# Kernel tuning notes

Measured on AMD Instinct MI355X. Metric: run time of the kernel, lower is better.

Reference implementation:

```python
import jax, jax.numpy as jnp
import numpy as np

P = 32    # num_particles
B = 64    # batch_size
T = 100   # seq_len
W = 50    # window_length
E = 64    # act embedding dim (emb_obs=0)
H = 256   # hidden_dim
ALPHA = 0.5  # resamp_alpha


def setup_inputs() -> dict:
    key = jax.random.key(0)
    ks = jax.random.split(key, 12)
    def lin(k, fan_in, shape):
        return jax.random.normal(k, shape, jnp.float32) / np.sqrt(fan_in).astype(np.float32)
    u = jax.random.uniform(ks[4], (T, B, P, P), jnp.float32, 1e-6, 1.0 - 1e-6)
    return {
        "prev_window": jax.random.normal(ks[0], (B, T, W), jnp.float32),
        "h0": jax.random.uniform(ks[1], (P * B, H), jnp.float32),
        "c0": jax.random.uniform(ks[2], (P * B, H), jnp.float32),
        "eps": jax.random.normal(ks[3], (T, P * B, H), jnp.float32),
        "gumbel": -jnp.log(-jnp.log(u)),  # Gumbel noise for multinomial resampling
        "W_act": lin(ks[5], W, (W, E)), "b_act": jnp.zeros((E,), jnp.float32),
        "W_ih": lin(ks[6], E, (E, 5 * H)), "b_ih": jnp.zeros((5 * H,), jnp.float32),
        "W_hh": lin(ks[7], H, (H, 5 * H)), "b_hh": jnp.zeros((5 * H,), jnp.float32),
        "W_obs": lin(ks[8], H + E, (H + E, 1)), "b_obs": jnp.zeros((1,), jnp.float32),
        "W_lab": lin(ks[9], H, (H, 1)), "b_lab": jnp.zeros((1,), jnp.float32),
    }


def reference(prev_window, h0, c0, eps, gumbel, W_act, b_act, W_ih, b_ih,
              W_hh, b_hh, W_obs, b_obs, W_lab, b_lab):
    # act embedding, tiled over particles (particle-major, matching torch repeat)
    emb = jax.nn.relu(prev_window @ W_act + b_act)          # [B,T,E]
    xs = jnp.swapaxes(jnp.tile(emb, (P, 1, 1)), 0, 1)       # [T,P*B,E]
    p0 = jnp.full((P * B, 1), np.log(1.0 / P), jnp.float32)

    barange = jnp.arange(B)

    def step(carry, inputs):
        h, c, p = carry                                      # [PB,H],[PB,H],[PB,1]
        x, eps_t, g_t = inputs                               # [PB,E],[PB,H],[B,P,P]
        gates = x @ W_ih + b_ih + h @ W_hh + b_hh            # [PB,5H]
        i, f, g, o, var = jnp.split(gates, 5, axis=1)
        mu = jax.nn.sigmoid(f) * c + jax.nn.sigmoid(i) * jnp.tanh(g)
        c1 = mu + jax.nn.softplus(var) * eps_t               # stochastic cell (reparameterize)
        h1 = jax.nn.sigmoid(o) * jnp.tanh(c1)
        # observation log-likelihood per particle
        logpdf = jnp.concatenate([h1, x], axis=1) @ W_obs + b_obs  # [PB,1]
        p1 = jax.nn.log_softmax((p + logpdf).reshape(P, B), axis=0)  # [P,B]
        # soft resampling: q = alpha*w + (1-alpha)/P, sample via Gumbel-argmax
        w1 = jnp.exp(p1)
        logits = jnp.log(ALPHA * w1 + (1.0 - ALPHA) / P)     # [P_src,B]
        idx = jnp.argmax(logits.T[:, None, :] + g_t, axis=-1).T  # [P_new,B]
        h_new = h1.reshape(P, B, H)[idx, barange[None, :]]   # [P,B,H]
        c_new = c1.reshape(P, B, H)[idx, barange[None, :]]
        w = w1[idx, barange[None, :]]                        # [P,B]
        w = w / (ALPHA * w + (1.0 - ALPHA) / P)              # importance correction
        p_new = jax.nn.log_softmax(jnp.log(w), axis=0)
        h_new = h_new.reshape(P * B, H)
        c_new = c_new.reshape(P * B, H)
        p_new = p_new.reshape(P * B, 1)
        return (h_new, c_new, p_new), (h_new, p_new)

    _, (hs, ps) = jax.lax.scan(step, (h0, c0, p0), (xs, eps, gumbel))
    # hs: [T,PB,H], ps: [T,PB,1]; dropout rate 0 -> identity
    prob = ps.reshape(T, P, B, 1)
    out = hs.reshape(T, P, B, H)
    y = jnp.sum(out * jnp.exp(prob), axis=1)                 # weighted particle mean [T,B,H]
    y_out = jax.nn.sigmoid(y @ W_lab + b_lab)                # [T,B,1]
    pf_out = jax.nn.sigmoid(hs @ W_lab + b_lab)              # [T,PB,1]
    return y_out, pf_out
```

## Files before the change

### kernel.cpp

```cpp
#include <hip/hip_runtime.h>
#include <hip/hip_bf16.h>
#include <cstddef>
#include <cstdint>

#define PP 32
#define BB 64
#define TT 100
#define WW 50
#define EE 64
#define HH 256

typedef float f4 __attribute__((ext_vector_type(4)));
typedef __attribute__((ext_vector_type(8))) short short8;
typedef __attribute__((ext_vector_type(4))) float f32x4;

__device__ __forceinline__ float sigm(float x) { return 1.0f / (1.0f + expf(-x)); }
__device__ __forceinline__ float splus(float x) {
    return fmaxf(x, 0.0f) + log1pf(expf(-fabsf(x)));
}
__device__ __forceinline__ unsigned short bfh(float x) {
    __hip_bfloat16 h = __float2bfloat16(x);
    return *reinterpret_cast<unsigned short*>(&h);
}
__device__ __forceinline__ float bff(unsigned short u) {
    __hip_bfloat16 h; *reinterpret_cast<unsigned short*>(&h) = u;
    return __bfloat162float(h);
}

__global__ __launch_bounds__(256) void k_emb(
    const float* __restrict__ pw, const float* __restrict__ w_act,
    const float* __restrict__ b_act, const float* __restrict__ w_obs,
    const float* __restrict__ b_obs,
    unsigned short* __restrict__ embh, unsigned short* __restrict__ embl,
    float* __restrict__ xobs)
{
    int tid = threadIdx.x;
    int sub = tid >> 6;
    int e   = tid & 63;
    int bt  = blockIdx.x * 4 + sub;
    int b = bt / TT, t = bt % TT;

    __shared__ float pws[4][WW + 2];
    if (e < WW) pws[sub][e] = pw[(size_t)bt * WW + e];
    __syncthreads();

    float acc = b_act[e];
    #pragma unroll 5
    for (int w = 0; w < WW; ++w) acc += pws[sub][w] * w_act[w * EE + e];
    float r = fmaxf(acc, 0.0f);

    unsigned short uh = bfh(r);
    embh[((size_t)t * BB + b) * EE + e] = uh;
    embl[((size_t)t * BB + b) * EE + e] = bfh(r - bff(uh));

    float xv = r * w_obs[HH + e];
    #pragma unroll
    for (int d = 1; d < 64; d <<= 1) xv += __shfl_xor(xv, d);
    if (e == 0) xobs[t * BB + b] = xv + b_obs[0];
}

__global__ __launch_bounds__(256) void k_packB(
    const float* __restrict__ W_ih, const float* __restrict__ W_hh,
    unsigned short* __restrict__ Bp)
{
    int i = blockIdx.x * 256 + threadIdx.x;
    int colp = i / 51200;  int r = i - colp * 51200;
    int bidx = r / 2560;   r -= bidx * 2560;
    int g    = r / 512;    r -= g * 512;
    int lane = r >> 3;     int e = r & 7;

    int c = (bidx < 10) ? bidx : (bidx - 10);
    int k = c * 32 + (lane >> 4) * 8 + e;
    int col = g * HH + colp * 16 + (lane & 15);
    float w = (k < HH) ? W_hh[(size_t)k * 1280 + col]
                       : W_ih[(size_t)(k - HH) * 1280 + col];
    unsigned short uh = bfh(w);
    Bp[i] = (bidx < 10) ? uh : bfh(w - bff(uh));
}

__global__ __launch_bounds__(256) void k_split0(
    const float* __restrict__ h0, const float* __restrict__ c0,
    unsigned short* __restrict__ hh, unsigned short* __restrict__ hl,
    float* __restrict__ cc)
{
    int i = blockIdx.x * 256 + threadIdx.x;
    float v = h0[i];
    unsigned short uh = bfh(v);
    hh[i] = uh;
    hl[i] = bfh(v - bff(uh));
    cc[i] = c0[i];
}

__global__ __launch_bounds__(256, 2) void s1_mfma(
    const unsigned short* __restrict__ Bp,
    const unsigned short* __restrict__ embh_t, const unsigned short* __restrict__ embl_t,
    const unsigned short* __restrict__ hh_in, const unsigned short* __restrict__ hl_in,
    const float* __restrict__ c_in,
    unsigned short* __restrict__ hh_out, unsigned short* __restrict__ hl_out,
    float* __restrict__ c_out,
    const int* __restrict__ gidx,
    const float* __restrict__ b_ih, const float* __restrict__ b_hh,
    const float* __restrict__ w_obs, const float* __restrict__ w_lab,
    const float* __restrict__ eps_t,
    float* __restrict__ dpo, float* __restrict__ dpl)
{
    const int tid  = threadIdx.x;
    const int rp   = blockIdx.x >> 4;
    const int cp   = blockIdx.x & 15;
    const int lane = tid & 63;
    const int w    = tid >> 6;
    const int lh   = lane & 15;
    const int kq   = lane >> 4;
    const int R0   = rp * 64 + w * 16;

    const int myrow = R0 + lh;
    const int sr    = gidx ? gidx[myrow] : myrow;
    const size_t hoff = (size_t)sr * 512 + (size_t)kq * 16;
    const size_t eoff = (size_t)(myrow & 63) * 128 + (size_t)kq * 16;

    f32x4 acc[5];
    #pragma unroll
    for (int g = 0; g < 5; ++g) acc[g] = (f32x4)(0.0f);

    const char* hhp = (const char*)hh_in  + hoff;
    const char* hlp = (const char*)hl_in  + hoff;
    const char* ehp = (const char*)embh_t + eoff;
    const char* elp = (const char*)embl_t + eoff;
    const short8* bslab = (const short8*)Bp + (size_t)cp * 6400 + lane;

    #pragma unroll
    for (int cs = 0; cs < 10; ++cs) {
        short8 Ah, Al;
        if (cs < 8) {
            Ah = *(const short8*)(hhp + cs * 64);
            Al = *(const short8*)(hlp + cs * 64);
        } else {
            Ah = *(const short8*)(ehp + (cs - 8) * 64);
            Al = *(const short8*)(elp + (cs - 8) * 64);
        }
        short8 Bh[5], Bl[5];
        #pragma unroll
        for (int g = 0; g < 5; ++g) {
            Bh[g] = bslab[(cs * 5 + g) * 64];
            Bl[g] = bslab[((cs + 10) * 5 + g) * 64];
        }
        #pragma unroll
        for (int g = 0; g < 5; ++g)
            acc[g] = __builtin_amdgcn_mfma_f32_16x16x32_bf16(Ah, Bh[g], acc[g], 0, 0, 0);
        #pragma unroll
        for (int g = 0; g < 5; ++g)
            acc[g] = __builtin_amdgcn_mfma_f32_16x16x32_bf16(Ah, Bl[g], acc[g], 0, 0, 0);
        #pragma unroll
        for (int g = 0; g < 5; ++g)
            acc[g] = __builtin_amdgcn_mfma_f32_16x16x32_bf16(Al, Bh[g], acc[g], 0, 0, 0);
    }

    const int hcol = cp * 16 + lh;
    float bsum[5];
    #pragma unroll
    for (int g = 0; g < 5; ++g) bsum[g] = b_ih[g * HH + hcol] + b_hh[g * HH + hcol];
    const float wobs_l = w_obs[hcol];
    const float wlab_l = w_lab[hcol];

    #pragma unroll
    for (int reg = 0; reg < 4; ++reg) {
        int row = R0 + kq * 4 + reg;
        int sr2 = gidx ? gidx[row] : row;
        float cpv = c_in[(size_t)sr2 * HH + hcol];
        float ep  = eps_t[(size_t)row * HH + hcol];

        float gi = acc[0][reg] + bsum[0];
        float gf = acc[1][reg] + bsum[1];
        float gg = acc[2][reg] + bsum[2];
        float go = acc[3][reg] + bsum[3];
        float gv = acc[4][reg] + bsum[4];

        float mu  = sigm(gf) * cpv + sigm(gi) * tanhf(gg);
        float c1v = mu + splus(gv) * ep;
        float h1v = sigm(go) * tanhf(c1v);

        c_out[(size_t)row * HH + hcol] = c1v;
        unsigned short uh = bfh(h1v);
        hh_out[(size_t)row * HH + hcol] = uh;
        hl_out[(size_t)row * HH + hcol] = bfh(h1v - bff(uh));

        float po = h1v * wobs_l, pl = h1v * wlab_l;
        po += __shfl_xor(po, 1); po += __shfl_xor(po, 2);
        po += __shfl_xor(po, 4); po += __shfl_xor(po, 8);
        pl += __shfl_xor(pl, 1); pl += __shfl_xor(pl, 2);
        pl += __shfl_xor(pl, 4); pl += __shfl_xor(pl, 8);
        if (lh == 0) {
            dpo[cp * 2048 + row] = po;
            dpl[cp * 2048 + row] = pl;
        }
    }
}

__global__ __launch_bounds__(256) void s2_kernel(
    const float* __restrict__ dpo, const float* __restrict__ dpl,
    const float* __restrict__ xobs_t, const float* __restrict__ g_t,
    const float* __restrict__ b_lab,
    float* __restrict__ p_buf, int first,
    int* __restrict__ gidx_next,
    float* __restrict__ y_out_t, float* __restrict__ pf_out_t)
{
    int b   = blockIdx.x;
    int tid = threadIdx.x;

    __shared__ float gt[PP][PP + 1];
    __shared__ float lg[PP];
    __shared__ float w1s[PP];
    __shared__ float lgt[PP];
    __shared__ float pnew[PP];
    __shared__ float dpart[PP];
    __shared__ int   idxs[PP];

    {
        f4 v = ((const f4*)(g_t + (size_t)b * 1024))[tid];
        int p = tid >> 3, j0 = (tid & 7) * 4;
        gt[p][j0 + 0] = v.x; gt[p][j0 + 1] = v.y;
        gt[p][j0 + 2] = v.z; gt[p][j0 + 3] = v.w;
    }

    int p = tid >> 3, j = tid & 7;
    {
        int o = p * BB + b;
        float s = dpo[j * 2048 + o] + dpo[(j + 8) * 2048 + o];
        s += __shfl_xor(s, 1); s += __shfl_xor(s, 2); s += __shfl_xor(s, 4);
        if (j == 0) {
            float pprev = first ? -3.4657359027997265f : p_buf[o];
            lg[p] = pprev + s + xobs_t[b];
        }
    }
    __syncthreads();

    if (tid < 32) {
        float v = lg[tid];
        float m = v;
        #pragma unroll
        for (int d = 1; d < 32; d <<= 1) m = fmaxf(m, __shfl_xor(m, d));
        float e = expf(v - m), se = e;
        #pragma unroll
        for (int d = 1; d < 32; d <<= 1) se += __shfl_xor(se, d);
        float l1 = v - m - logf(se);
        float w1 = expf(l1);
        w1s[tid] = w1;
        lgt[tid] = logf(0.5f * w1 + 0.015625f);
    }
    __syncthreads();

    if (tid < 32) {
        int p2 = tid;
        float best = -INFINITY; int bi = 0;
        #pragma unroll 8
        for (int jj = 0; jj < 32; ++jj) {
            float val = lgt[jj] + gt[p2][jj];
            if (val > best) { best = val; bi = jj; }
        }
        idxs[p2] = bi;
        gidx_next[p2 * BB + b] = bi * BB + b;

        float wv = w1s[bi];
        wv = wv / (0.5f * wv + 0.015625f);
        float lw = logf(wv);
        float m2 = lw;
        #pragma unroll
        for (int d = 1; d < 32; d <<= 1) m2 = fmaxf(m2, __shfl_xor(m2, d));
        float e2 = expf(lw - m2), s2 = e2;
        #pragma unroll
        for (int d = 1; d < 32; d <<= 1) s2 += __shfl_xor(s2, d);
        float pn = lw - m2 - logf(s2);
        pnew[p2] = pn;
        p_buf[p2 * BB + b] = pn;
    }
    __syncthreads();

    {
        int src = idxs[p] * BB + b;
        float d = dpl[j * 2048 + src] + dpl[(j + 8) * 2048 + src];
        d += __shfl_xor(d, 1); d += __shfl_xor(d, 2); d += __shfl_xor(d, 4);
        if (j == 0) dpart[p] = d;
    }
    __syncthreads();

    if (tid < 32) {
        float dd = dpart[tid];
        float bl = b_lab[0];
        pf_out_t[tid * BB + b] = 1.0f / (1.0f + expf(-(dd + bl)));
        float contrib = expf(pnew[tid]) * dd;
        #pragma unroll
        for (int d = 1; d < 32; d <<= 1) contrib += __shfl_xor(contrib, d);
        if (tid == 0) y_out_t[b] = 1.0f / (1.0f + expf(-(contrib + bl)));
    }
}

extern "C" void kernel_launch(void* const* d_in, const int* in_sizes, int n_in,
                              void* d_out, int out_size, void* d_ws, size_t ws_size,
                              hipStream_t stream)
{
    const float* prev_window = (const float*)d_in[0];
    const float* h0    = (const float*)d_in[1];
    const float* c0    = (const float*)d_in[2];
    const float* eps   = (const float*)d_in[3];
    const float* gum   = (const float*)d_in[4];
    const float* W_act = (const float*)d_in[5];
    const float* b_act = (const float*)d_in[6];
    const float* W_ih  = (const float*)d_in[7];
    const float* b_ih  = (const float*)d_in[8];
    const float* W_hh  = (const float*)d_in[9];
    const float* b_hh  = (const float*)d_in[10];
    const float* W_obs = (const float*)d_in[11];
    const float* b_obs = (const float*)d_in[12];
    const float* W_lab = (const float*)d_in[13];
    const float* b_lab = (const float*)d_in[14];

    float* out = (float*)d_out;
    char* w = (char*)d_ws;

    unsigned short* Bp   = (unsigned short*)(w);
    unsigned short* embh = (unsigned short*)(w + 1638400);
    unsigned short* embl = (unsigned short*)(w + 2457600);
    unsigned short* hhA  = (unsigned short*)(w + 3276800);
    unsigned short* hlA  = (unsigned short*)(w + 4325376);
    unsigned short* hhB  = (unsigned short*)(w + 5373952);
    unsigned short* hlB  = (unsigned short*)(w + 6422528);
    float*  cA   = (float*)(w + 7471104);
    float*  cB   = (float*)(w + 9568256);
    float*  xobs = (float*)(w + 11665408);
    float*  pbuf = (float*)(w + 11691008);
    int*    gidx = (int*)(w + 11699200);
    float*  dpo  = (float*)(w + 11707392);
    float*  dpl  = (float*)(w + 11838464);

    k_emb<<<1600, 256, 0, stream>>>(prev_window, W_act, b_act, W_obs, b_obs,
                                    embh, embl, xobs);
    k_packB<<<3200, 256, 0, stream>>>(W_ih, W_hh, Bp);
    k_split0<<<2048, 256, 0, stream>>>(h0, c0, hhA, hlA, cA);

    for (int t = 0; t < TT; ++t) {
        const unsigned short* hh_in = (t & 1) ? hhB : hhA;
        const unsigned short* hl_in = (t & 1) ? hlB : hlA;
        const float*          c_in  = (t & 1) ? cB  : cA;
        unsigned short* hh_out = (t & 1) ? hhA : hhB;
        unsigned short* hl_out = (t & 1) ? hlA : hlB;
        float*          c_out  = (t & 1) ? cA  : cB;

        s1_mfma<<<512, 256, 0, stream>>>(
            Bp, embh + (size_t)t * 4096, embl + (size_t)t * 4096,
            hh_in, hl_in, c_in, hh_out, hl_out, c_out,
            (t == 0) ? nullptr : gidx,
            b_ih, b_hh, W_obs, W_lab,
            eps + (size_t)t * 524288,
            dpo, dpl);

        s2_kernel<<<64, 256, 0, stream>>>(
            dpo, dpl, xobs + t * BB, gum + (size_t)t * 65536,
            b_lab, pbuf, (t == 0) ? 1 : 0, gidx,
            out + (size_t)t * BB,
            out + (size_t)TT * BB + (size_t)t * PP * BB);
    }
}
```

Measured before the change: 2.648 ms.

## Compute two 16-row fragments per wave to reuse B loads in s1_mfma

Each wave now handles 32 rows (two 16-row MFMA fragments) instead of 16, so every B-slab load feeds twice as many MFMAs. The grid drops from 512 to 256 blocks and launch bounds relax to one block per SM to make room for the doubled accumulators. The goal is to halve the redundant weight traffic, at the cost of fewer waves to hide latency across the 256 CUs.

```diff
diff --git a/kernel.cpp b/kernel.cpp
--- a/kernel.cpp
+++ b/kernel.cpp
@@ -91,7 +91,7 @@
     cc[i] = c0[i];
 }
 
-__global__ __launch_bounds__(256, 2) void s1_mfma(
+__global__ __launch_bounds__(256, 1) void s1_mfma(
     const unsigned short* __restrict__ Bp,
     const unsigned short* __restrict__ embh_t, const unsigned short* __restrict__ embl_t,
     const unsigned short* __restrict__ hh_in, const unsigned short* __restrict__ hl_in,
@@ -105,38 +105,47 @@
     float* __restrict__ dpo, float* __restrict__ dpl)
 {
     const int tid  = threadIdx.x;
-    const int rp   = blockIdx.x >> 4;
+    const int rgrp = blockIdx.x >> 4;
     const int cp   = blockIdx.x & 15;
     const int lane = tid & 63;
     const int w    = tid >> 6;
     const int lh   = lane & 15;
     const int kq   = lane >> 4;
-    const int R0   = rp * 64 + w * 16;
-
-    const int myrow = R0 + lh;
-    const int sr    = gidx ? gidx[myrow] : myrow;
-    const size_t hoff = (size_t)sr * 512 + (size_t)kq * 16;
-    const size_t eoff = (size_t)(myrow & 63) * 128 + (size_t)kq * 16;
-
-    f32x4 acc[5];
-    #pragma unroll
-    for (int g = 0; g < 5; ++g) acc[g] = (f32x4)(0.0f);
-
-    const char* hhp = (const char*)hh_in  + hoff;
-    const char* hlp = (const char*)hl_in  + hoff;
-    const char* ehp = (const char*)embh_t + eoff;
-    const char* elp = (const char*)embl_t + eoff;
+    const int rg   = rgrp * 4 + w;
+    const int R0   = rg * 32;
+
+    size_t hoff[2], eoff[2];
+    #pragma unroll
+    for (int fr = 0; fr < 2; ++fr) {
+        int myrow = R0 + fr * 16 + lh;
+        int sr    = gidx ? gidx[myrow] : myrow;
+        hoff[fr] = (size_t)sr * 512 + (size_t)kq * 16;
+        eoff[fr] = (size_t)(myrow & 63) * 128 + (size_t)kq * 16;
+    }
+
+    f32x4 acc0[5], acc1[5];
+    #pragma unroll
+    for (int g = 0; g < 5; ++g) { acc0[g] = (f32x4)(0.0f); acc1[g] = (f32x4)(0.0f); }
+
+    const char* hhp = (const char*)hh_in;
+    const char* hlp = (const char*)hl_in;
+    const char* ehp = (const char*)embh_t;
+    const char* elp = (const char*)embl_t;
     const short8* bslab = (const short8*)Bp + (size_t)cp * 6400 + lane;
 
     #pragma unroll
     for (int cs = 0; cs < 10; ++cs) {
-        short8 Ah, Al;
+        short8 Ah0, Al0, Ah1, Al1;
         if (cs < 8) {
-            Ah = *(const short8*)(hhp + cs * 64);
-            Al = *(const short8*)(hlp + cs * 64);
+            Ah0 = *(const short8*)(hhp + hoff[0] + cs * 64);
+            Al0 = *(const short8*)(hlp + hoff[0] + cs * 64);
+            Ah1 = *(const short8*)(hhp + hoff[1] + cs * 64);
+            Al1 = *(const short8*)(hlp + hoff[1] + cs * 64);
         } else {
-            Ah = *(const short8*)(ehp + (cs - 8) * 64);
-            Al = *(const short8*)(elp + (cs - 8) * 64);
+            Ah0 = *(const short8*)(ehp + eoff[0] + (cs - 8) * 64);
+            Al0 = *(const short8*)(elp + eoff[0] + (cs - 8) * 64);
+            Ah1 = *(const short8*)(ehp + eoff[1] + (cs - 8) * 64);
+            Al1 = *(const short8*)(elp + eoff[1] + (cs - 8) * 64);
         }
         short8 Bh[5], Bl[5];
         #pragma unroll
@@ -145,14 +154,20 @@
             Bl[g] = bslab[((cs + 10) * 5 + g) * 64];
         }
         #pragma unroll
-        for (int g = 0; g < 5; ++g)
-            acc[g] = __builtin_amdgcn_mfma_f32_16x16x32_bf16(Ah, Bh[g], acc[g], 0, 0, 0);
-        #pragma unroll
-        for (int g = 0; g < 5; ++g)
-            acc[g] = __builtin_amdgcn_mfma_f32_16x16x32_bf16(Ah, Bl[g], acc[g], 0, 0, 0);
-        #pragma unroll
-        for (int g = 0; g < 5; ++g)
-            acc[g] = __builtin_amdgcn_mfma_f32_16x16x32_bf16(Al, Bh[g], acc[g], 0, 0, 0);
+        for (int g = 0; g < 5; ++g) {
+            acc0[g] = __builtin_amdgcn_mfma_f32_16x16x32_bf16(Ah0, Bh[g], acc0[g], 0, 0, 0);
+            acc1[g] = __builtin_amdgcn_mfma_f32_16x16x32_bf16(Ah1, Bh[g], acc1[g], 0, 0, 0);
+        }
+        #pragma unroll
+        for (int g = 0; g < 5; ++g) {
+            acc0[g] = __builtin_amdgcn_mfma_f32_16x16x32_bf16(Ah0, Bl[g], acc0[g], 0, 0, 0);
+            acc1[g] = __builtin_amdgcn_mfma_f32_16x16x32_bf16(Ah1, Bl[g], acc1[g], 0, 0, 0);
+        }
+        #pragma unroll
+        for (int g = 0; g < 5; ++g) {
+            acc0[g] = __builtin_amdgcn_mfma_f32_16x16x32_bf16(Al0, Bh[g], acc0[g], 0, 0, 0);
+            acc1[g] = __builtin_amdgcn_mfma_f32_16x16x32_bf16(Al1, Bh[g], acc1[g], 0, 0, 0);
+        }
     }
 
     const int hcol = cp * 16 + lh;
@@ -163,35 +178,39 @@
     const float wlab_l = w_lab[hcol];
 
     #pragma unroll
-    for (int reg = 0; reg < 4; ++reg) {
-        int row = R0 + kq * 4 + reg;
-        int sr2 = gidx ? gidx[row] : row;
-        float cpv = c_in[(size_t)sr2 * HH + hcol];
-        float ep  = eps_t[(size_t)row * HH + hcol];
-
-        float gi = acc[0][reg] + bsum[0];
-        float gf = acc[1][reg] + bsum[1];
-        float gg = acc[2][reg] + bsum[2];
-        float go = acc[3][reg] + bsum[3];
-        float gv = acc[4][reg] + bsum[4];
-
-        float mu  = sigm(gf) * cpv + sigm(gi) * tanhf(gg);
-        float c1v = mu + splus(gv) * ep;
-        float h1v = sigm(go) * tanhf(c1v);
-
-        c_out[(size_t)row * HH + hcol] = c1v;
-        unsigned short uh = bfh(h1v);
-        hh_out[(size_t)row * HH + hcol] = uh;
-        hl_out[(size_t)row * HH + hcol] = bfh(h1v - bff(uh));
-
-        float po = h1v * wobs_l, pl = h1v * wlab_l;
-        po += __shfl_xor(po, 1); po += __shfl_xor(po, 2);
-        po += __shfl_xor(po, 4); po += __shfl_xor(po, 8);
-        pl += __shfl_xor(pl, 1); pl += __shfl_xor(pl, 2);
-        pl += __shfl_xor(pl, 4); pl += __shfl_xor(pl, 8);
-        if (lh == 0) {
-            dpo[cp * 2048 + row] = po;
-            dpl[cp * 2048 + row] = pl;
+    for (int fr = 0; fr < 2; ++fr) {
+        #pragma unroll
+        for (int reg = 0; reg < 4; ++reg) {
+            int row = R0 + fr * 16 + kq * 4 + reg;
+            int sr2 = gidx ? gidx[row] : row;
+            float cpv = c_in[(size_t)sr2 * HH + hcol];
+            float ep  = eps_t[(size_t)row * HH + hcol];
+
+            const f32x4* ac = fr ? acc1 : acc0;
+            float gi = ac[0][reg] + bsum[0];
+            float gf = ac[1][reg] + bsum[1];
+            float gg = ac[2][reg] + bsum[2];
+            float go = ac[3][reg] + bsum[3];
+            float gv = ac[4][reg] + bsum[4];
+
+            float mu  = sigm(gf) * cpv + sigm(gi) * tanhf(gg);
+            float c1v = mu + splus(gv) * ep;
+            float h1v = sigm(go) * tanhf(c1v);
+
+            c_out[(size_t)row * HH + hcol] = c1v;
+            unsigned short uh = bfh(h1v);
+            hh_out[(size_t)row * HH + hcol] = uh;
+            hl_out[(size_t)row * HH + hcol] = bfh(h1v - bff(uh));
+
+            float po = h1v * wobs_l, pl = h1v * wlab_l;
+            po += __shfl_xor(po, 1); po += __shfl_xor(po, 2);
+            po += __shfl_xor(po, 4); po += __shfl_xor(po, 8);
+            pl += __shfl_xor(pl, 1); pl += __shfl_xor(pl, 2);
+            pl += __shfl_xor(pl, 4); pl += __shfl_xor(pl, 8);
+            if (lh == 0) {
+                dpo[cp * 2048 + row] = po;
+                dpl[cp * 2048 + row] = pl;
+            }
         }
     }
 }
@@ -345,7 +364,7 @@
         unsigned short* hl_out = (t & 1) ? hlA : hlB;
         float*          c_out  = (t & 1) ? cA  : cB;
 
-        s1_mfma<<<512, 256, 0, stream>>>(
+        s1_mfma<<<256, 256, 0, stream>>>(
             Bp, embh + (size_t)t * 4096, embl + (size_t)t * 4096,
             hh_in, hl_in, c_in, hh_out, hl_out, c_out,
             (t == 0) ? nullptr : gidx,
```

Result: slower. 2.757 ms (+4.1%).
